# Kernel tuning notes

Hardware: AMD Instinct MI355X
Metric: run time of the kernel (lower is better)

Reference implementation:

```python
import jax, jax.numpy as jnp
import numpy as np

EPS = 1e-7  # keras_backend.epsilon()
ROUTINGS = 3


def setup_inputs() -> dict:
    key = jax.random.key(0)
    k1, k2, k3, k4, k5 = jax.random.split(key, 5)
    B, H, W, I, O = 32, 8, 8, 32, 64
    return {
        "inputs_poses": jax.random.normal(k1, (B, H, W, I, 4, 4), dtype=jnp.float32),
        "inputs_activations": jax.random.uniform(k2, (B, H, W, I), dtype=jnp.float32),
        "w": jax.random.normal(k3, (I, O, 4, 4), dtype=jnp.float32),
        "beta_v": jax.random.normal(k4, (1, O), dtype=jnp.float32),
        "beta_a": jax.random.normal(k5, (1, O), dtype=jnp.float32),
    }


def _em_routing(votes, i_act, beta_v, beta_a, routings):
    # votes: [B, N, O, 16], i_act: [B, N]
    B, N, O, P = votes.shape
    act = i_act[..., None, None]              # [B, N, 1, 1]
    bv = beta_v[..., None, :, None]           # [1, 1, O, 1]
    ba = beta_a[..., None, :, None]           # [1, 1, O, 1]
    rr = jnp.full((N, O, 1), 1.0 / O, dtype=votes.dtype)
    it_min, it_max = 1.0, min(routings, 3.0)
    o_mean = o_act = None
    for it in range(routings):
        inv_temp = it_min + (it_max - it_min) * it / max(1.0, routings - 1.0)
        # ---- m-step ----
        rr_prime = rr * act                                    # [B, N, O, 1]
        rps = rr_prime.sum(axis=-3, keepdims=True)             # [B, 1, O, 1]
        o_mean = (rr_prime * votes).sum(axis=-3, keepdims=True) / rps   # [B,1,O,16]
        o_stdv = jnp.sqrt((rr_prime * jnp.square(votes - o_mean)).sum(axis=-3, keepdims=True) / rps)
        o_cost_h = (bv + jnp.log(o_stdv + EPS)) * rps          # [B,1,O,16]
        o_cost = o_cost_h.sum(axis=-1, keepdims=True)          # [B,1,O,1]
        o_cost_mean = o_cost.mean(axis=-2, keepdims=True)      # [B,1,1,1]
        o_cost_stdv = jnp.sqrt(jnp.square(o_cost - o_cost_mean).sum(axis=-2, keepdims=True) / O)
        o_act = jax.nn.sigmoid(inv_temp * (ba + (o_cost_mean - o_cost) / (o_cost_stdv + EPS)))
        # ---- e-step ----
        if it < routings - 1:
            o_p = (-jnp.sum(jnp.square(votes - o_mean) / (2.0 * jnp.square(o_stdv)), axis=-1, keepdims=True)
                   - jnp.sum(jnp.log(o_stdv + EPS), axis=-1, keepdims=True))   # [B,N,O,1]
            zz = jnp.log(o_act + EPS) + o_p
            rr = jax.nn.softmax(zz, axis=-2)                   # softmax over O
    poses = jnp.squeeze(o_mean, axis=-3)                       # [B, O, 16]
    activations = jnp.squeeze(o_act, axis=(-3, -1))            # [B, O]
    return poses, activations


def reference(inputs_poses, inputs_activations, w, beta_v, beta_a):
    B, H, W, I = inputs_activations.shape
    O = w.shape[1]
    # mat_transform: per-(input-type, class) 4x4 pose transform -> votes
    pose = inputs_poses.reshape(B * H * W, I, 4, 4)
    votes = jnp.einsum('siab,iobc->sioac', pose, w)            # [BHW, I, O, 4, 4]
    votes = votes.reshape(B, H, W, I, O, 16)
    # coord_addition: add scaled spatial coords to components 0 (h) and 1 (w)
    ch = jnp.zeros((1, H, 1, 1, 1, 16), votes.dtype).at[..., 0].set(
        ((jnp.arange(H, dtype=votes.dtype) + 0.5) / H).reshape(1, H, 1, 1, 1))
    cw = jnp.zeros((1, 1, W, 1, 1, 16), votes.dtype).at[..., 1].set(
        ((jnp.arange(W, dtype=votes.dtype) + 0.5) / W).reshape(1, 1, W, 1, 1))
    votes = votes + ch + cw
    votes = votes.reshape(B, H * W * I, O, 16)
    i_act = inputs_activations.reshape(B, H * W * I)
    poses, activations = _em_routing(votes, i_act, beta_v, beta_a, ROUTINGS)
    poses = poses.reshape(B, O, 4, 4)
    return poses, activations
```

## Files before the change

### kernel.cpp

```cpp
#include <hip/hip_runtime.h>


#define NB 32
#define NN 2048
#define NO 64
#define NP 16
#define EPSF 1e-7f

#define SITES_PB 8
#define IS_PB 16
#define PAIRS_PB (SITES_PB * IS_PB)

#define ACC_SLOTS 33
#define ACC_PER_B (ACC_SLOTS * NO)
#define ACC_TOTAL (NB * ACC_PER_B)

template <bool FIRST>
__global__ __launch_bounds__(1024) void accum_kernel(
    const float* __restrict__ pose,
    const float* __restrict__ act,
    const float* __restrict__ wmat,
    const float* __restrict__ beta_v,
    const float* __restrict__ beta_a,
    const float* __restrict__ accum_prev,
    float* __restrict__ accum_out,
    float inv_temp)
{
    __shared__ float pose_s[PAIRS_PB * 16];
    __shared__ float act_s[PAIRS_PB];
    __shared__ float stats_s[ACC_PER_B];
    __shared__ float buf[4][ACC_PER_B];

    const int b = blockIdx.y;
    const int sg = blockIdx.x >> 1;
    const int ig = blockIdx.x & 1;
    const int s0 = sg * SITES_PB;
    const int tid = threadIdx.x;
    const int w = tid >> 6;
    const int o = tid & 63;
    const int i = ig * 16 + w;
    const int grp = w >> 2, wvin = w & 3;

    const float4* wp = (const float4*)(wmat + ((size_t)i * 64 + o) * 16);
    float4 w0 = wp[0], w1 = wp[1], w2 = wp[2], w3 = wp[3];

    if (tid < PAIRS_PB * 4) {
        const int pr = tid >> 2, qw = tid & 3;
        const int sl = pr >> 4, li = pr & 15;
        const size_t n = (size_t)b * NN + (s0 + sl) * 32 + ig * 16 + li;
        ((float4*)pose_s)[pr * 4 + qw] = ((const float4*)(pose + n * 16))[qw];
    } else if (tid < PAIRS_PB * 4 + PAIRS_PB) {
        const int t = tid - PAIRS_PB * 4;
        const int sl = t >> 4, li = t & 15;
        act_s[t] = act[(size_t)b * NN + (s0 + sl) * 32 + ig * 16 + li];
    }

    if (!FIRST && tid < 64) {
        const float* ap = accum_prev + (size_t)b * ACC_PER_B;
        float rps = ap[32 * 64 + o];
        float rinv = 1.0f / rps;
        float logsum = 0.f;
        float mm[16], vv[16];
        #pragma unroll
        for (int p = 0; p < 16; p++) {
            float mv = ap[p * 64 + o] * rinv;
            float va = fmaxf(ap[(16 + p) * 64 + o] * rinv - mv * mv, 0.f);
            mm[p] = mv;
            vv[p] = va;
            logsum += __logf(sqrtf(va) + EPSF);
        }
        float cost = rps * (16.0f * beta_v[o] + logsum);
        float cm = cost;
        #pragma unroll
        for (int s = 32; s > 0; s >>= 1) cm += __shfl_xor(cm, s, 64);
        cm *= (1.0f / 64.0f);
        float dd = cost - cm;
        float cs = dd * dd;
        #pragma unroll
        for (int s = 32; s > 0; s >>= 1) cs += __shfl_xor(cs, s, 64);
        cs = sqrtf(cs * (1.0f / 64.0f));
        float x = inv_temp * (beta_a[o] + (cm - cost) / (cs + EPSF));
        float oa = 1.0f / (1.0f + __expf(-x));
        #pragma unroll
        for (int p = 0; p < 16; p++) stats_s[p * 64 + o] = mm[p];
        #pragma unroll
        for (int p = 0; p < 16; p++) stats_s[(16 + p) * 64 + o] = 0.5f / vv[p];
        stats_s[32 * 64 + o] = __logf(oa + EPSF) - logsum;
    }
    __syncthreads();

    float m[16], i2v[16], zzb = 0.f;
    if (!FIRST) {
        #pragma unroll
        for (int p = 0; p < 16; p++) m[p] = stats_s[p * 64 + o];
        #pragma unroll
        for (int p = 0; p < 16; p++) i2v[p] = stats_s[(16 + p) * 64 + o];
        zzb = stats_s[32 * 64 + o];
    }

    float accR = 0.f, acc1[16], acc2[16];
    #pragma unroll
    for (int p = 0; p < 16; p++) { acc1[p] = 0.f; acc2[p] = 0.f; }

    for (int sl = 0; sl < 8; sl++) {
        const int site = s0 + sl;
        const float c0 = ((site >> 3) + 0.5f) * 0.125f;
        const float c1 = ((site & 7) + 0.5f) * 0.125f;
        const float* pr = pose_s + (sl * 16 + w) * 16;

        float v[16];
        #pragma unroll
        for (int a = 0; a < 4; a++) {
            float pa0 = pr[a * 4 + 0], pa1 = pr[a * 4 + 1];
            float pa2 = pr[a * 4 + 2], pa3 = pr[a * 4 + 3];
            v[a * 4 + 0] = pa0 * w0.x + pa1 * w1.x + pa2 * w2.x + pa3 * w3.x;
            v[a * 4 + 1] = pa0 * w0.y + pa1 * w1.y + pa2 * w2.y + pa3 * w3.y;
            v[a * 4 + 2] = pa0 * w0.z + pa1 * w1.z + pa2 * w2.z + pa3 * w3.z;
            v[a * 4 + 3] = pa0 * w0.w + pa1 * w1.w + pa2 * w2.w + pa3 * w3.w;
        }
        v[0] += c0;
        v[1] += c1;

        float rr;
        if (FIRST) {
            rr = 1.0f / 64.0f;
        } else {
            float d = zzb;
            #pragma unroll
            for (int p = 0; p < 16; p++) {
                float t = v[p] - m[p];
                d -= t * t * i2v[p];
            }
            float mx = d;
            #pragma unroll
            for (int s = 32; s > 0; s >>= 1) mx = fmaxf(mx, __shfl_xor(mx, s, 64));
            float e = __expf(d - mx);
            float sum = e;
            #pragma unroll
            for (int s = 32; s > 0; s >>= 1) sum += __shfl_xor(sum, s, 64);
            rr = e / sum;
        }
        float rp = rr * act_s[sl * 16 + w];
        accR += rp;
        #pragma unroll
        for (int p = 0; p < 16; p++) {
            acc1[p] += rp * v[p];
            acc2[p] += rp * v[p] * v[p];
        }
    }

    if (wvin == 3) {
        float* r = buf[grp];
        r[32 * 64 + o] = accR;
        #pragma unroll
        for (int p = 0; p < 16; p++) r[p * 64 + o] = acc1[p];
        #pragma unroll
        for (int p = 0; p < 16; p++) r[(16 + p) * 64 + o] = acc2[p];
    }
    __syncthreads();
    if (wvin == 2) {
        float* r = buf[grp];
        r[32 * 64 + o] += accR;
        #pragma unroll
        for (int p = 0; p < 16; p++) r[p * 64 + o] += acc1[p];
        #pragma unroll
        for (int p = 0; p < 16; p++) r[(16 + p) * 64 + o] += acc2[p];
    }
    __syncthreads();
    if (wvin == 1) {
        float* r = buf[grp];
        r[32 * 64 + o] += accR;
        #pragma unroll
        for (int p = 0; p < 16; p++) r[p * 64 + o] += acc1[p];
        #pragma unroll
        for (int p = 0; p < 16; p++) r[(16 + p) * 64 + o] += acc2[p];
    }
    __syncthreads();
    if (wvin == 0) {
        float* r = buf[grp];
        r[32 * 64 + o] += accR;
        #pragma unroll
        for (int p = 0; p < 16; p++) r[p * 64 + o] += acc1[p];
        #pragma unroll
        for (int p = 0; p < 16; p++) r[(16 + p) * 64 + o] += acc2[p];
    }
    __syncthreads();

    float* ac = accum_out + (size_t)b * ACC_PER_B;
    for (int j = tid; j < ACC_PER_B; j += 1024)
        atomicAdd(ac + j, buf[0][j] + buf[1][j] + buf[2][j] + buf[3][j]);
}

__global__ __launch_bounds__(64) void stats_final(
    const float* __restrict__ accum,
    const float* __restrict__ beta_v,
    const float* __restrict__ beta_a,
    float* __restrict__ out,
    float inv_temp)
{
    const int b = blockIdx.x;
    const int o = threadIdx.x;
    const float* ac = accum + (size_t)b * ACC_PER_B;

    float rps = ac[32 * 64 + o];
    float rinv = 1.0f / rps;
    float m[16];
    float logsum = 0.f;
    #pragma unroll
    for (int p = 0; p < 16; p++) {
        float mm = ac[p * 64 + o] * rinv;
        float vv = fmaxf(ac[(16 + p) * 64 + o] * rinv - mm * mm, 0.f);
        m[p] = mm;
        logsum += __logf(sqrtf(vv) + EPSF);
    }
    float cost = rps * (16.0f * beta_v[o] + logsum);

    float cm = cost;
    #pragma unroll
    for (int s = 32; s > 0; s >>= 1) cm += __shfl_xor(cm, s, 64);
    cm *= (1.0f / 64.0f);
    float dd = cost - cm;
    float cs = dd * dd;
    #pragma unroll
    for (int s = 32; s > 0; s >>= 1) cs += __shfl_xor(cs, s, 64);
    cs = sqrtf(cs * (1.0f / 64.0f));

    float x = inv_temp * (beta_a[o] + (cm - cost) / (cs + EPSF));
    float oa = 1.0f / (1.0f + __expf(-x));

    float* op = out + ((size_t)b * 64 + o) * 16;
    #pragma unroll
    for (int p = 0; p < 16; p++) op[p] = m[p];
    out[(size_t)NB * NO * NP + (size_t)b * 64 + o] = oa;
}

extern "C" void kernel_launch(void* const* d_in, const int* in_sizes, int n_in,
                              void* d_out, int out_size, void* d_ws, size_t ws_size,
                              hipStream_t stream) {
    const float* pose   = (const float*)d_in[0];
    const float* act    = (const float*)d_in[1];
    const float* wmat   = (const float*)d_in[2];
    const float* beta_v = (const float*)d_in[3];
    const float* beta_a = (const float*)d_in[4];
    float* out = (float*)d_out;
    float* ws = (float*)d_ws;

    float* a0 = ws;
    float* a1 = ws + (size_t)ACC_TOTAL;
    float* a2 = ws + 2 * (size_t)ACC_TOTAL;

    hipMemsetAsync(ws, 0, 3 * (size_t)ACC_TOTAL * sizeof(float), stream);

    dim3 grid(16, NB);
    accum_kernel<true ><<<grid, 1024, 0, stream>>>(pose, act, wmat, beta_v, beta_a,
                                                   nullptr, a0, 0.0f);
    accum_kernel<false><<<grid, 1024, 0, stream>>>(pose, act, wmat, beta_v, beta_a,
                                                   a0, a1, 1.0f);
    accum_kernel<false><<<grid, 1024, 0, stream>>>(pose, act, wmat, beta_v, beta_a,
                                                   a1, a2, 2.0f);
    stats_final<<<NB, 64, 0, stream>>>(a2, beta_v, beta_a, out, 3.0f);
}
```

Baseline: 156.3 us.

## Read poses directly from global memory and drop per-pair softmax max reduction

```diff
diff --git a/kernel.cpp b/kernel.cpp
--- a/kernel.cpp
+++ b/kernel.cpp
@@ -9,7 +9,6 @@
 
 #define SITES_PB 8
 #define IS_PB 16
-#define PAIRS_PB (SITES_PB * IS_PB)
 
 #define ACC_SLOTS 33
 #define ACC_PER_B (ACC_SLOTS * NO)
@@ -26,8 +25,6 @@
     float* __restrict__ accum_out,
     float inv_temp)
 {
-    __shared__ float pose_s[PAIRS_PB * 16];
-    __shared__ float act_s[PAIRS_PB];
     __shared__ float stats_s[ACC_PER_B];
     __shared__ float buf[4][ACC_PER_B];
 
@@ -44,17 +41,6 @@
     const float4* wp = (const float4*)(wmat + ((size_t)i * 64 + o) * 16);
     float4 w0 = wp[0], w1 = wp[1], w2 = wp[2], w3 = wp[3];
 
-    if (tid < PAIRS_PB * 4) {
-        const int pr = tid >> 2, qw = tid & 3;
-        const int sl = pr >> 4, li = pr & 15;
-        const size_t n = (size_t)b * NN + (s0 + sl) * 32 + ig * 16 + li;
-        ((float4*)pose_s)[pr * 4 + qw] = ((const float4*)(pose + n * 16))[qw];
-    } else if (tid < PAIRS_PB * 4 + PAIRS_PB) {
-        const int t = tid - PAIRS_PB * 4;
-        const int sl = t >> 4, li = t & 15;
-        act_s[t] = act[(size_t)b * NN + (s0 + sl) * 32 + ig * 16 + li];
-    }
-
     if (!FIRST && tid < 64) {
         const float* ap = accum_prev + (size_t)b * ACC_PER_B;
         float rps = ap[32 * 64 + o];
@@ -81,42 +67,51 @@
         cs = sqrtf(cs * (1.0f / 64.0f));
         float x = inv_temp * (beta_a[o] + (cm - cost) / (cs + EPSF));
         float oa = 1.0f / (1.0f + __expf(-x));
+        float zzb = __logf(oa + EPSF) - logsum;
+        float K = zzb;
+        #pragma unroll
+        for (int s = 32; s > 0; s >>= 1) K = fmaxf(K, __shfl_xor(K, s, 64));
         #pragma unroll
         for (int p = 0; p < 16; p++) stats_s[p * 64 + o] = mm[p];
         #pragma unroll
         for (int p = 0; p < 16; p++) stats_s[(16 + p) * 64 + o] = 0.5f / vv[p];
-        stats_s[32 * 64 + o] = __logf(oa + EPSF) - logsum;
-    }
-    __syncthreads();
-
-    float m[16], i2v[16], zzb = 0.f;
+        stats_s[32 * 64 + o] = zzb - K;
+    }
+    __syncthreads();
+
+    float m[16], i2v[16], zzbK = 0.f;
     if (!FIRST) {
         #pragma unroll
         for (int p = 0; p < 16; p++) m[p] = stats_s[p * 64 + o];
         #pragma unroll
         for (int p = 0; p < 16; p++) i2v[p] = stats_s[(16 + p) * 64 + o];
-        zzb = stats_s[32 * 64 + o];
+        zzbK = stats_s[32 * 64 + o];
     }
 
     float accR = 0.f, acc1[16], acc2[16];
     #pragma unroll
     for (int p = 0; p < 16; p++) { acc1[p] = 0.f; acc2[p] = 0.f; }
+
+    const int base_n = __builtin_amdgcn_readfirstlane(s0 * 32 + ig * 16 + w);
+    const float* pose_b = pose + (size_t)b * NN * 16;
+    const float* act_b  = act + (size_t)b * NN;
 
     for (int sl = 0; sl < 8; sl++) {
         const int site = s0 + sl;
         const float c0 = ((site >> 3) + 0.5f) * 0.125f;
         const float c1 = ((site & 7) + 0.5f) * 0.125f;
-        const float* pr = pose_s + (sl * 16 + w) * 16;
+        const int n = base_n + sl * 32;
+        const float4* pr4 = (const float4*)(pose_b + (size_t)n * 16);
+        const float av = act_b[n];
 
         float v[16];
         #pragma unroll
         for (int a = 0; a < 4; a++) {
-            float pa0 = pr[a * 4 + 0], pa1 = pr[a * 4 + 1];
-            float pa2 = pr[a * 4 + 2], pa3 = pr[a * 4 + 3];
-            v[a * 4 + 0] = pa0 * w0.x + pa1 * w1.x + pa2 * w2.x + pa3 * w3.x;
-            v[a * 4 + 1] = pa0 * w0.y + pa1 * w1.y + pa2 * w2.y + pa3 * w3.y;
-            v[a * 4 + 2] = pa0 * w0.z + pa1 * w1.z + pa2 * w2.z + pa3 * w3.z;
-            v[a * 4 + 3] = pa0 * w0.w + pa1 * w1.w + pa2 * w2.w + pa3 * w3.w;
+            float4 pa = pr4[a];
+            v[a * 4 + 0] = pa.x * w0.x + pa.y * w1.x + pa.z * w2.x + pa.w * w3.x;
+            v[a * 4 + 1] = pa.x * w0.y + pa.y * w1.y + pa.z * w2.y + pa.w * w3.y;
+            v[a * 4 + 2] = pa.x * w0.z + pa.y * w1.z + pa.z * w2.z + pa.w * w3.z;
+            v[a * 4 + 3] = pa.x * w0.w + pa.y * w1.w + pa.z * w2.w + pa.w * w3.w;
         }
         v[0] += c0;
         v[1] += c1;
@@ -125,22 +120,19 @@
         if (FIRST) {
             rr = 1.0f / 64.0f;
         } else {
-            float d = zzb;
+            float d = zzbK;
             #pragma unroll
             for (int p = 0; p < 16; p++) {
                 float t = v[p] - m[p];
                 d -= t * t * i2v[p];
             }
-            float mx = d;
-            #pragma unroll
-            for (int s = 32; s > 0; s >>= 1) mx = fmaxf(mx, __shfl_xor(mx, s, 64));
-            float e = __expf(d - mx);
+            float e = __expf(d);
             float sum = e;
             #pragma unroll
             for (int s = 32; s > 0; s >>= 1) sum += __shfl_xor(sum, s, 64);
-            rr = e / sum;
-        }
-        float rp = rr * act_s[sl * 16 + w];
+            rr = e / fmaxf(sum, 1e-30f);
+        }
+        float rp = rr * av;
         accR += rp;
         #pragma unroll
         for (int p = 0; p < 16; p++) {
```

Result: faster. 146.7 us (-6.1%).
